# Performance work log

Measured on AMD Instinct MI355X. Metric: run time of the kernel, lower is better.

Reference implementation:

```python
import jax, jax.numpy as jnp
import numpy as np

E = 1024
H = 16
D = E // H
NUM_BUCKETS = 320
MAX_DISTANCE = 800


def _relative_positions_bucket(relative_positions):
    # relative_positions: int32 [T, S]
    num_buckets = NUM_BUCKETS // 2  # 160
    relative_buckets = (relative_positions > 0).astype(jnp.int32) * num_buckets
    rel = jnp.abs(relative_positions)
    max_exact = num_buckets // 2  # 80
    is_small = rel < max_exact
    rel_f = jnp.maximum(rel, 1).astype(jnp.float32)
    large = jnp.log(rel_f / max_exact) / np.log(MAX_DISTANCE / max_exact) * (num_buckets - max_exact)
    large = (max_exact + large).astype(jnp.int32)
    large = jnp.minimum(large, num_buckets - 1)
    relative_buckets = relative_buckets + jnp.where(is_small, rel, large)
    return relative_buckets


def setup_inputs() -> dict:
    key = jax.random.key(0)
    ks = jax.random.split(key, 12)
    B, T = 2, 2048
    s = 0.02
    return {
        "hidden_states": jax.random.normal(ks[0], (B, T, E), dtype=jnp.float32),
        "q_w": jax.random.normal(ks[1], (E, E), dtype=jnp.float32) * s,
        "q_b": jnp.zeros((E,), dtype=jnp.float32),
        "k_w": jax.random.normal(ks[2], (E, E), dtype=jnp.float32) * s,
        "k_b": jnp.zeros((E,), dtype=jnp.float32),
        "v_w": jax.random.normal(ks[3], (E, E), dtype=jnp.float32) * s,
        "v_b": jnp.zeros((E,), dtype=jnp.float32),
        "out_w": jax.random.normal(ks[4], (E, E), dtype=jnp.float32) * s,
        "out_b": jnp.zeros((E,), dtype=jnp.float32),
        "rel_embed": jax.random.normal(ks[5], (NUM_BUCKETS, H), dtype=jnp.float32) * s,
        "gru_const": jnp.ones((1, H, 1, 1), dtype=jnp.float32),
        "gru_w": jax.random.normal(ks[6], (8, D), dtype=jnp.float32) * s,
        "gru_b": jnp.zeros((8,), dtype=jnp.float32),
    }


def reference(hidden_states, q_w, q_b, k_w, k_b, v_w, v_b, out_w, out_b,
              rel_embed, gru_const, gru_w, gru_b):
    B, T, _ = hidden_states.shape
    scaling = D ** (-0.5)

    # --- relative position bias: [H, T, T] ---
    ctx = jnp.arange(T, dtype=jnp.int32)[:, None]
    mem = jnp.arange(T, dtype=jnp.int32)[None, :]
    buckets = _relative_positions_bucket(mem - ctx)          # [T, T]
    position_bias = rel_embed[buckets]                        # [T, T, H]
    position_bias = jnp.transpose(position_bias, (2, 0, 1))   # [H, T, T]

    # --- gate (gru_rel_pos): per (b, h, t) scalar ---
    gated = hidden_states.reshape(B, T, H, D).transpose(0, 2, 1, 3)  # [B,H,T,D]
    proj = jnp.einsum('bhtd,ed->bhte', gated, gru_w) + gru_b         # [B,H,T,8]
    proj = proj.reshape(B, H, T, 2, 4).sum(-1)                        # [B,H,T,2]
    gate = jax.nn.sigmoid(proj)
    gate_a = gate[..., 0:1]
    gate_b = gate[..., 1:2]
    gate_out = gate_a * (gate_b * gru_const - 1.0) + 2.0              # [B,H,T,1]
    gated_position_bias = gate_out * position_bias[None]              # [B,H,T,T]

    # --- attention (same math as F.multi_head_attention_forward eager path) ---
    q = (hidden_states @ q_w.T + q_b).reshape(B, T, H, D).transpose(0, 2, 1, 3) * scaling
    k = (hidden_states @ k_w.T + k_b).reshape(B, T, H, D).transpose(0, 2, 1, 3)
    v = (hidden_states @ v_w.T + v_b).reshape(B, T, H, D).transpose(0, 2, 1, 3)

    scores = jnp.einsum('bhtd,bhsd->bhts', q, k) + gated_position_bias
    attn = jax.nn.softmax(scores, axis=-1)
    ctx_out = jnp.einsum('bhts,bhsd->bhtd', attn, v)                  # [B,H,T,D]
    ctx_out = ctx_out.transpose(0, 2, 1, 3).reshape(B, T, E)
    return ctx_out @ out_w.T + out_b
```

## Files before the change

kernel.cpp:

```cpp
#include <hip/hip_runtime.h>
#include <hip/hip_bf16.h>
#include <math.h>

typedef __bf16 bf16;
typedef __bf16 bf16x4 __attribute__((ext_vector_type(4)));
typedef __bf16 bf16x8 __attribute__((ext_vector_type(8)));
typedef float  f32x4  __attribute__((ext_vector_type(4)));
typedef unsigned u32x2 __attribute__((ext_vector_type(2)));
typedef unsigned u32x4 __attribute__((ext_vector_type(4)));

#define T_SEQ 2048
#define E_DIM 1024
#define H_NUM 16
#define D_DIM 64
#define NDELTA 4095
#define LOG2E 1.4426950408889634f

__device__ __forceinline__ void gld16(const bf16* g, bf16* l) {
  __builtin_amdgcn_global_load_lds((__attribute__((address_space(1))) void*)(g),
                                   (__attribute__((address_space(3))) void*)(l), 16, 0, 0);
}

__device__ __forceinline__ void qswap(unsigned &a, unsigned &b) {
  u32x2 t  = __builtin_amdgcn_permlane32_swap(a, b, false, false);
  u32x2 t2 = __builtin_amdgcn_permlane16_swap(t[0], t[1], false, false);
  a = t2[0]; b = t2[1];
}

__global__ __launch_bounds__(256)
void cast_gate_kernel(const float* __restrict__ hs, bf16* __restrict__ hsb,
                      const float* __restrict__ gru_w, const float* __restrict__ gru_b,
                      const float* __restrict__ gconst, float* __restrict__ gate)
{
  __shared__ float w[512];
  const int tid = threadIdx.x;
  const int bt  = blockIdx.x;
  w[tid]       = gru_w[tid];
  w[tid + 256] = gru_w[tid + 256];
  __syncthreads();

  const int i = bt * 256 + tid;
  const float4 xv = reinterpret_cast<const float4*>(hs)[i];
  bf16x4 o;
  o[0] = (bf16)xv.x; o[1] = (bf16)xv.y; o[2] = (bf16)xv.z; o[3] = (bf16)xv.w;
  reinterpret_cast<bf16x4*>(hsb)[i] = o;

  const int h  = tid >> 4;
  const int d0 = (tid & 15) * 4;
  float acc[8];
#pragma unroll
  for (int e = 0; e < 8; e++) {
    acc[e] = xv.x * w[e*64+d0] + xv.y * w[e*64+d0+1]
           + xv.z * w[e*64+d0+2] + xv.w * w[e*64+d0+3];
  }
#pragma unroll
  for (int e = 0; e < 8; e++) {
    float v = acc[e];
    v += __shfl_xor(v, 1);
    v += __shfl_xor(v, 2);
    v += __shfl_xor(v, 4);
    v += __shfl_xor(v, 8);
    acc[e] = v;
  }
  if ((tid & 15) == 0) {
    float p0 = acc[0]+acc[1]+acc[2]+acc[3] + gru_b[0]+gru_b[1]+gru_b[2]+gru_b[3];
    float p1 = acc[4]+acc[5]+acc[6]+acc[7] + gru_b[4]+gru_b[5]+gru_b[6]+gru_b[7];
    float ga = 1.0f / (1.0f + expf(-p0));
    float gb = 1.0f / (1.0f + expf(-p1));
    float g = (ga * (gb * gconst[h] - 1.0f) + 2.0f) * LOG2E;
    int bb = bt >> 11;
    int t  = bt & (T_SEQ - 1);
    gate[((size_t)(bb * H_NUM + h)) * T_SEQ + t] = g;
  }
}

__global__ void cast_w_kernel(const float* __restrict__ q_w, const float* __restrict__ k_w,
                              const float* __restrict__ v_w, const float* __restrict__ o_w,
                              bf16* __restrict__ wcat, bf16* __restrict__ wob,
                              const float* __restrict__ rel_embed, float* __restrict__ pbt) {
  int sel = blockIdx.y;
  int tid = threadIdx.x;
  if (sel == 4) {
    int dd = blockIdx.x * 256 + tid;
    if (blockIdx.x >= 16 || dd >= NDELTA) return;
    int delta = dd - (T_SEQ - 1);
    int bucket = (delta > 0) ? 160 : 0;
    int rel = abs(delta);
    int v;
    if (rel < 80) {
      v = rel;
    } else {
      float rf = (float)(rel < 1 ? 1 : rel);
      float lf = logf(rf / 80.0f) * (80.0f / 2.302585092994046f);
      int lg = 80 + (int)lf;
      v = lg < 159 ? lg : 159;
    }
    bucket += v;
#pragma unroll
    for (int h = 0; h < H_NUM; h++)
      pbt[h * NDELTA + dd] = rel_embed[bucket * H_NUM + h];
    return;
  }
  int i = blockIdx.x * 256 + tid;
  const float* src = (sel == 0) ? q_w : (sel == 1) ? k_w : (sel == 2) ? v_w : o_w;
  bf16* dst = (sel < 3) ? (wcat + (size_t)sel * 1048576) : wob;
  const float4 v = reinterpret_cast<const float4*>(src)[i];
  bf16x4 o;
  o[0] = (bf16)v.x; o[1] = (bf16)v.y; o[2] = (bf16)v.z; o[3] = (bf16)v.w;
  reinterpret_cast<bf16x4*>(dst)[i] = o;
}

template<int MODE, int N_TOTAL>
__global__ __launch_bounds__(256)
void gemm2_kernel(const bf16* __restrict__ A, const bf16* __restrict__ W,
                  const float* __restrict__ b0, const float* __restrict__ b1,
                  const float* __restrict__ b2, float qalpha,
                  void* __restrict__ out0, void* __restrict__ out1, void* __restrict__ out2)
{
  __shared__ bf16 As[128 * 64];
  __shared__ bf16 Bs[128 * 64];
  const int tid  = threadIdx.x;
  const int lane = tid & 63;
  const int wave = tid >> 6;
  const int m0 = blockIdx.y * 128;
  const int n0 = blockIdx.x * 128;
  const int wm = (wave >> 1) * 64;
  const int wn = (wave & 1) * 64;
  const int qd = lane >> 4;
  const int lm = lane & 15;

  const int srow8  = lane >> 3;
  const int schunk = ((lane & 7) ^ srow8) * 8;
  const bf16* gA = A + (size_t)(m0 + wave * 32 + srow8) * 1024 + schunk;
  const bf16* gB = W + (size_t)(n0 + wave * 32 + srow8) * 1024 + schunk;
  bf16* lA = As + wave * 32 * 64;
  bf16* lB = Bs + wave * 32 * 64;

  f32x4 acc[4][4] = {};
  const int xs = lm & 7;

  for (int k0 = 0; k0 < 1024; k0 += 64) {
#pragma unroll
    for (int j = 0; j < 4; j++) {
      gld16(gA + (size_t)j * 8 * 1024 + k0, lA + j * 8 * 64);
      gld16(gB + (size_t)j * 8 * 1024 + k0, lB + j * 8 * 64);
    }
    __syncthreads();
    bf16x8 af[4][2], bfr[4][2];
#pragma unroll
    for (int i = 0; i < 4; i++) {
#pragma unroll
      for (int kk = 0; kk < 2; kk++) {
        af[i][kk]  = *(const bf16x8*)&As[(wm + i * 16 + lm) * 64 + (((kk * 4 + qd) ^ xs) * 8)];
        bfr[i][kk] = *(const bf16x8*)&Bs[(wn + i * 16 + lm) * 64 + (((kk * 4 + qd) ^ xs) * 8)];
      }
    }
#pragma unroll
    for (int kk = 0; kk < 2; kk++)
#pragma unroll
      for (int im = 0; im < 4; im++)
#pragma unroll
        for (int in = 0; in < 4; in++)
          acc[im][in] = __builtin_amdgcn_mfma_f32_16x16x32_bf16(af[im][kk], bfr[in][kk], acc[im][in], 0, 0, 0);
    __syncthreads();
  }

  const int seg = n0 >> 10;
  const float* bias = (MODE == 0) ? b0 : (seg == 0 ? b0 : (seg == 1 ? b1 : b2));
  const float alpha = (MODE == 1 && seg == 0) ? qalpha : 1.0f;

#pragma unroll
  for (int im = 0; im < 4; im++) {
#pragma unroll
    for (int in = 0; in < 4; in++) {
      const int n  = n0 + wn + in * 16 + lm;
      const int n1 = n & 1023;
      const float bv = bias[n1];
      const int mb = m0 + wm + im * 16 + qd * 4;
      if (MODE == 0) {
        float* o = (float*)out0;
#pragma unroll
        for (int r = 0; r < 4; r++)
          o[(size_t)(mb + r) * 1024 + n1] = acc[im][in][r] + bv;
      } else if (seg == 2) {
        const int bb = mb >> 11;
        const int t  = mb & 2047;
        bf16x4 pk;
#pragma unroll
        for (int r = 0; r < 4; r++) pk[r] = (bf16)(acc[im][in][r] + bv);
        *(bf16x4*)&((bf16*)out2)[((size_t)(bb * 1024 + n1)) * 2048 + t] = pk;
      } else {
        bf16* o = (bf16*)(seg == 0 ? out0 : out1);
#pragma unroll
        for (int r = 0; r < 4; r++)
          o[(size_t)(mb + r) * 1024 + n1] = (bf16)((acc[im][in][r] + bv) * alpha);
      }
    }
  }
}

__global__ __launch_bounds__(256)
void gemm_o_kernel(const bf16* __restrict__ A, const bf16* __restrict__ W,
                   const float* __restrict__ bias, float* __restrict__ out)
{
  __shared__ bf16 As[64 * 32];
  __shared__ bf16 Bs[128 * 32];
  const int tid  = threadIdx.x;
  const int lane = tid & 63;
  const int wave = tid >> 6;
  const int m0 = blockIdx.y * 64;
  const int n0 = blockIdx.x * 128;
  const int wm = (wave >> 1) * 32;
  const int wn = (wave & 1) * 64;
  const int qd = lane >> 4;
  const int lm = lane & 15;

  const int row4 = lane >> 2;
  const int col8 = (lane & 3) * 8;
  const bf16* gA0 = A + (size_t)(m0 + wave * 16 + row4) * 1024 + col8;
  const bf16* gB0 = W + (size_t)(n0 + wave * 32 + row4) * 1024 + col8;
  const bf16* gB1 = gB0 + (size_t)16 * 1024;
  bf16* lA0 = As + wave * 16 * 32;
  bf16* lB0 = Bs + (wave * 2 + 0) * 512;
  bf16* lB1 = Bs + (wave * 2 + 1) * 512;

  f32x4 acc[2][4] = {};

  for (int k0 = 0; k0 < 1024; k0 += 32) {
    gld16(gA0 + k0, lA0);
    gld16(gB0 + k0, lB0);
    gld16(gB1 + k0, lB1);
    __syncthreads();
    bf16x8 af[2], bfr[4];
#pragma unroll
    for (int i = 0; i < 2; i++)
      af[i]  = *(const bf16x8*)&As[(wm + i * 16 + lm) * 32 + qd * 8];
#pragma unroll
    for (int i = 0; i < 4; i++)
      bfr[i] = *(const bf16x8*)&Bs[(wn + i * 16 + lm) * 32 + qd * 8];
#pragma unroll
    for (int im = 0; im < 2; im++)
#pragma unroll
      for (int in = 0; in < 4; in++)
        acc[im][in] = __builtin_amdgcn_mfma_f32_16x16x32_bf16(af[im], bfr[in], acc[im][in], 0, 0, 0);
    __syncthreads();
  }

#pragma unroll
  for (int im = 0; im < 2; im++) {
#pragma unroll
    for (int in = 0; in < 4; in++) {
      const int n  = n0 + wn + in * 16 + lm;
      const float bv = bias[n];
      const int mb = m0 + wm + im * 16 + qd * 4;
#pragma unroll
      for (int r = 0; r < 4; r++)
        out[(size_t)(mb + r) * 1024 + n] = acc[im][in][r] + bv;
    }
  }
}

#define LK 72
__global__ __launch_bounds__(256)
void attn3_kernel(const bf16* __restrict__ Qg, const bf16* __restrict__ Kg,
                  const bf16* __restrict__ Vtg, const float* __restrict__ gate,
                  const float* __restrict__ pbt, bf16* __restrict__ ctx)
{
  __shared__ bf16 Ks[2][64 * LK];
  __shared__ bf16 Vs[2][64 * LK];
  __shared__ float pbs[2176];

  const int t0 = blockIdx.x * 128;
  const int h  = blockIdx.y;
  const int b  = blockIdx.z;
  const int tid  = threadIdx.x;
  const int lane = tid & 63;
  const int wave = tid >> 6;
  const int qd = lane >> 4;
  const int lm = lane & 15;

  for (int i = tid; i < 2176; i += 256) {
    int idx = i - t0 + 1920;
    pbs[i] = (idx >= 0 && idx < NDELTA) ? pbt[h * NDELTA + idx] : 0.0f;
  }

  bf16x8 qf[2][2];
  float g[2];
#pragma unroll
  for (int nb = 0; nb < 2; nb++) {
    const int q = t0 + wave * 32 + nb * 16 + lm;
    const bf16* qrow = Qg + (size_t)(b * T_SEQ + q) * E_DIM + h * D_DIM;
    qf[nb][0] = *(const bf16x8*)(qrow + qd * 8);
    qf[nb][1] = *(const bf16x8*)(qrow + 32 + qd * 8);
    g[nb] = gate[((size_t)(b * H_NUM + h)) * T_SEQ + q];
  }

  const int srow = tid >> 2;
  const int scol = (tid & 3) * 16;
  const bf16* kgp = Kg  + ((size_t)(b * T_SEQ) + srow) * E_DIM + h * D_DIM + scol;
  const bf16* vgp = Vtg + ((size_t)(b * 1024) + h * D_DIM + srow) * T_SEQ + scol;

  {
    bf16x8 a0 = *(const bf16x8*)kgp;
    bf16x8 a1 = *(const bf16x8*)(kgp + 8);
    bf16x8 c0 = *(const bf16x8*)vgp;
    bf16x8 c1 = *(const bf16x8*)(vgp + 8);
    *(bf16x8*)&Ks[0][srow * LK + scol]     = a0;
    *(bf16x8*)&Ks[0][srow * LK + scol + 8] = a1;
    *(bf16x8*)&Vs[0][srow * LK + scol]     = c0;
    *(bf16x8*)&Vs[0][srow * LK + scol + 8] = c1;
  }
  __syncthreads();

  f32x4 o[4][2] = {};
  float li[2] = {0.0f, 0.0f};

  for (int it = 0; it < T_SEQ / 64; it++) {
    const int s0 = it * 64;
    const int buf = it & 1;
    const bool more = (it + 1 < T_SEQ / 64);
    bf16x8 nk0, nk1, nv0, nv1;
    if (more) {
      const bf16* kn = kgp + (size_t)(s0 + 64) * E_DIM;
      const bf16* vn = vgp + (s0 + 64);
      nk0 = *(const bf16x8*)kn; nk1 = *(const bf16x8*)(kn + 8);
      nv0 = *(const bf16x8*)vn; nv1 = *(const bf16x8*)(vn + 8);
    }

    bf16x8 kf[4][2];
#pragma unroll
    for (int mb = 0; mb < 4; mb++) {
      kf[mb][0] = *(const bf16x8*)&Ks[buf][(16 * mb + lm) * LK + qd * 8];
      kf[mb][1] = *(const bf16x8*)&Ks[buf][(16 * mb + lm) * LK + 32 + qd * 8];
    }

    bf16x8 pf[2][2];
#pragma unroll
    for (int nb = 0; nb < 2; nb++) {
      f32x4 sc[4];
#pragma unroll
      for (int mb = 0; mb < 4; mb++) {
        f32x4 t = {};
        t = __builtin_amdgcn_mfma_f32_16x16x32_bf16(kf[mb][0], qf[nb][0], t, 0, 0, 0);
        t = __builtin_amdgcn_mfma_f32_16x16x32_bf16(kf[mb][1], qf[nb][1], t, 0, 0, 0);
        sc[mb] = t;
      }
      const int ib = s0 + 4 * qd + 127 - (wave * 32 + nb * 16 + lm);
      float rs = 0.0f;
      unsigned wlo[4], whi[4];
#pragma unroll
      for (int mb = 0; mb < 4; mb++) {
        bf16x4 pk;
#pragma unroll
        for (int r = 0; r < 4; r++) {
          float p = __builtin_amdgcn_exp2f(sc[mb][r] + g[nb] * pbs[ib + 16 * mb + r]);
          rs += p;
          pk[r] = (bf16)p;
        }
        u32x2 pw = __builtin_bit_cast(u32x2, pk);
        wlo[mb] = pw[0]; whi[mb] = pw[1];
      }
      li[nb] += rs;
      unsigned a0 = wlo[0], b0v = wlo[1], a1 = whi[0], b1v = whi[1];
      qswap(a0, b0v);
      qswap(a1, b1v);
      u32x4 h0; h0[0] = a0; h0[1] = a1; h0[2] = b0v; h0[3] = b1v;
      pf[nb][0] = __builtin_bit_cast(bf16x8, h0);
      unsigned c0 = wlo[2], d0v = wlo[3], c1 = whi[2], d1v = whi[3];
      qswap(c0, d0v);
      qswap(c1, d1v);
      u32x4 h1; h1[0] = c0; h1[1] = c1; h1[2] = d0v; h1[3] = d1v;
      pf[nb][1] = __builtin_bit_cast(bf16x8, h1);
    }

#pragma unroll
    for (int db = 0; db < 4; db++) {
      bf16x8 vf0 = *(const bf16x8*)&Vs[buf][(16 * db + lm) * LK + qd * 8];
      bf16x8 vf1 = *(const bf16x8*)&Vs[buf][(16 * db + lm) * LK + 32 + qd * 8];
#pragma unroll
      for (int nb = 0; nb < 2; nb++) {
        o[db][nb] = __builtin_amdgcn_mfma_f32_16x16x32_bf16(vf0, pf[nb][0], o[db][nb], 0, 0, 0);
        o[db][nb] = __builtin_amdgcn_mfma_f32_16x16x32_bf16(vf1, pf[nb][1], o[db][nb], 0, 0, 0);
      }
    }
    if (more) {
      *(bf16x8*)&Ks[buf ^ 1][srow * LK + scol]     = nk0;
      *(bf16x8*)&Ks[buf ^ 1][srow * LK + scol + 8] = nk1;
      *(bf16x8*)&Vs[buf ^ 1][srow * LK + scol]     = nv0;
      *(bf16x8*)&Vs[buf ^ 1][srow * LK + scol + 8] = nv1;
    }
    __syncthreads();
  }

#pragma unroll
  for (int nb = 0; nb < 2; nb++) {
    li[nb] += __shfl_xor(li[nb], 16);
    li[nb] += __shfl_xor(li[nb], 32);
  }
#pragma unroll
  for (int nb = 0; nb < 2; nb++) {
    const float inv = 1.0f / li[nb];
    const int q = t0 + wave * 32 + nb * 16 + lm;
    bf16* obase = ctx + (size_t)(b * T_SEQ + q) * E_DIM + h * D_DIM + 4 * qd;
#pragma unroll
    for (int db = 0; db < 4; db++) {
      bf16x4 ov;
      ov[0] = (bf16)(o[db][nb][0] * inv); ov[1] = (bf16)(o[db][nb][1] * inv);
      ov[2] = (bf16)(o[db][nb][2] * inv); ov[3] = (bf16)(o[db][nb][3] * inv);
      *(bf16x4*)&obase[16 * db] = ov;
    }
  }
}

extern "C" void kernel_launch(void* const* d_in, const int* in_sizes, int n_in,
                              void* d_out, int out_size, void* d_ws, size_t ws_size,
                              hipStream_t stream)
{
  const float* hs     = (const float*)d_in[0];
  const float* q_w    = (const float*)d_in[1];
  const float* q_b    = (const float*)d_in[2];
  const float* k_w    = (const float*)d_in[3];
  const float* k_b    = (const float*)d_in[4];
  const float* v_w    = (const float*)d_in[5];
  const float* v_b    = (const float*)d_in[6];
  const float* out_w  = (const float*)d_in[7];
  const float* out_b  = (const float*)d_in[8];
  const float* rel    = (const float*)d_in[9];
  const float* gconst = (const float*)d_in[10];
  const float* gru_w  = (const float*)d_in[11];
  const float* gru_b  = (const float*)d_in[12];

  char* p = (char*)d_ws;
  bf16* hsb  = (bf16*)p; p += (size_t)4096 * 1024 * 2;
  bf16* wcat = (bf16*)p; p += (size_t)3072 * 1024 * 2;
  bf16* wob  = (bf16*)p; p += (size_t)1024 * 1024 * 2;
  bf16* Qb   = (bf16*)p; p += (size_t)4096 * 1024 * 2;
  bf16* Kb   = (bf16*)p; p += (size_t)4096 * 1024 * 2;
  bf16* Vtb  = (bf16*)p; p += (size_t)2048 * 2048 * 2;
  bf16* ctxb = (bf16*)p; p += (size_t)4096 * 1024 * 2;
  float* gatep = (float*)p; p += (size_t)2 * H_NUM * T_SEQ * 4;
  float* pbt   = (float*)p; p += (size_t)H_NUM * NDELTA * 4;

  cast_gate_kernel<<<4096, 256, 0, stream>>>(hs, hsb, gru_w, gru_b, gconst, gatep);
  cast_w_kernel<<<dim3(1024, 5), 256, 0, stream>>>(q_w, k_w, v_w, out_w, wcat, wob, rel, pbt);

  const float qalpha = 0.125f * LOG2E;
  gemm2_kernel<1, 3072><<<dim3(24, 32), 256, 0, stream>>>(
      hsb, wcat, q_b, k_b, v_b, qalpha, Qb, Kb, Vtb);

  attn3_kernel<<<dim3(T_SEQ / 128, H_NUM, 2), 256, 0, stream>>>(Qb, Kb, Vtb, gatep, pbt, ctxb);

  gemm_o_kernel<<<dim3(8, 64), 256, 0, stream>>>(ctxb, wob, out_b, (float*)d_out);
}
```

Measured before the change: 219.7 us.

## Split attention KV loop across wave pairs and load K/V directly from global

The attention kernel doubles its block to 512 threads. Two groups of four waves each take alternating 64-key tiles and merge their partial outputs and row sums through shared memory at the end. The LDS double-buffered K/V staging and its per-iteration barriers are removed, and each wave now loads its MFMA operands straight from global memory (relying on L1/L2 for reuse). This removes the sync and LDS traffic and adds intra-block parallelism over the key dimension, at the cost of redundant global loads across waves and an exposed load latency with no explicit prefetch.

Result: slower. 289.1 us (+31.6%).

```diff
diff --git a/kernel.cpp b/kernel.cpp
--- a/kernel.cpp
+++ b/kernel.cpp
@@ -260,15 +260,14 @@
   }
 }
 
-#define LK 72
-__global__ __launch_bounds__(256)
+__global__ __launch_bounds__(512, 4)
 void attn3_kernel(const bf16* __restrict__ Qg, const bf16* __restrict__ Kg,
                   const bf16* __restrict__ Vtg, const float* __restrict__ gate,
                   const float* __restrict__ pbt, bf16* __restrict__ ctx)
 {
-  __shared__ bf16 Ks[2][64 * LK];
-  __shared__ bf16 Vs[2][64 * LK];
   __shared__ float pbs[2176];
+  __shared__ float oxf[4][64][36];
+  __shared__ float lixf[4][64][2];
 
   const int t0 = blockIdx.x * 128;
   const int h  = blockIdx.y;
@@ -276,10 +275,12 @@
   const int tid  = threadIdx.x;
   const int lane = tid & 63;
   const int wave = tid >> 6;
+  const int pw = wave & 3;
+  const int sh = wave >> 2;
   const int qd = lane >> 4;
   const int lm = lane & 15;
 
-  for (int i = tid; i < 2176; i += 256) {
+  for (int i = tid; i < 2176; i += 512) {
     int idx = i - t0 + 1920;
     pbs[i] = (idx >= 0 && idx < NDELTA) ? pbt[h * NDELTA + idx] : 0.0f;
   }
@@ -288,50 +289,36 @@
   float g[2];
 #pragma unroll
   for (int nb = 0; nb < 2; nb++) {
-    const int q = t0 + wave * 32 + nb * 16 + lm;
+    const int q = t0 + pw * 32 + nb * 16 + lm;
     const bf16* qrow = Qg + (size_t)(b * T_SEQ + q) * E_DIM + h * D_DIM;
     qf[nb][0] = *(const bf16x8*)(qrow + qd * 8);
     qf[nb][1] = *(const bf16x8*)(qrow + 32 + qd * 8);
     g[nb] = gate[((size_t)(b * H_NUM + h)) * T_SEQ + q];
   }
 
-  const int srow = tid >> 2;
-  const int scol = (tid & 3) * 16;
-  const bf16* kgp = Kg  + ((size_t)(b * T_SEQ) + srow) * E_DIM + h * D_DIM + scol;
-  const bf16* vgp = Vtg + ((size_t)(b * 1024) + h * D_DIM + srow) * T_SEQ + scol;
-
-  {
-    bf16x8 a0 = *(const bf16x8*)kgp;
-    bf16x8 a1 = *(const bf16x8*)(kgp + 8);
-    bf16x8 c0 = *(const bf16x8*)vgp;
-    bf16x8 c1 = *(const bf16x8*)(vgp + 8);
-    *(bf16x8*)&Ks[0][srow * LK + scol]     = a0;
-    *(bf16x8*)&Ks[0][srow * LK + scol + 8] = a1;
-    *(bf16x8*)&Vs[0][srow * LK + scol]     = c0;
-    *(bf16x8*)&Vs[0][srow * LK + scol + 8] = c1;
-  }
+  const bf16* krow[4];
+#pragma unroll
+  for (int mb = 0; mb < 4; mb++)
+    krow[mb] = Kg + ((size_t)(b * T_SEQ + 16 * mb + lm)) * E_DIM + h * D_DIM + qd * 8;
+  const bf16* vrow[4];
+#pragma unroll
+  for (int db = 0; db < 4; db++)
+    vrow[db] = Vtg + ((size_t)(b * 1024 + h * D_DIM + 16 * db + lm)) * T_SEQ + qd * 8;
+
   __syncthreads();
 
   f32x4 o[4][2] = {};
   float li[2] = {0.0f, 0.0f};
 
-  for (int it = 0; it < T_SEQ / 64; it++) {
+  for (int it = sh; it < T_SEQ / 64; it += 2) {
     const int s0 = it * 64;
-    const int buf = it & 1;
-    const bool more = (it + 1 < T_SEQ / 64);
-    bf16x8 nk0, nk1, nv0, nv1;
-    if (more) {
-      const bf16* kn = kgp + (size_t)(s0 + 64) * E_DIM;
-      const bf16* vn = vgp + (s0 + 64);
-      nk0 = *(const bf16x8*)kn; nk1 = *(const bf16x8*)(kn + 8);
-      nv0 = *(const bf16x8*)vn; nv1 = *(const bf16x8*)(vn + 8);
-    }
 
     bf16x8 kf[4][2];
 #pragma unroll
     for (int mb = 0; mb < 4; mb++) {
-      kf[mb][0] = *(const bf16x8*)&Ks[buf][(16 * mb + lm) * LK + qd * 8];
-      kf[mb][1] = *(const bf16x8*)&Ks[buf][(16 * mb + lm) * LK + 32 + qd * 8];
+      const bf16* kg = krow[mb] + (size_t)s0 * E_DIM;
+      kf[mb][0] = *(const bf16x8*)kg;
+      kf[mb][1] = *(const bf16x8*)(kg + 32);
     }
 
     bf16x8 pf[2][2];
@@ -345,7 +332,7 @@
         t = __builtin_amdgcn_mfma_f32_16x16x32_bf16(kf[mb][1], qf[nb][1], t, 0, 0, 0);
         sc[mb] = t;
       }
-      const int ib = s0 + 4 * qd + 127 - (wave * 32 + nb * 16 + lm);
+      const int ib = s0 + 4 * qd + 127 - (pw * 32 + nb * 16 + lm);
       float rs = 0.0f;
       unsigned wlo[4], whi[4];
 #pragma unroll
@@ -357,8 +344,8 @@
           rs += p;
           pk[r] = (bf16)p;
         }
-        u32x2 pw = __builtin_bit_cast(u32x2, pk);
-        wlo[mb] = pw[0]; whi[mb] = pw[1];
+        u32x2 pw2 = __builtin_bit_cast(u32x2, pk);
+        wlo[mb] = pw2[0]; whi[mb] = pw2[1];
       }
       li[nb] += rs;
       unsigned a0 = wlo[0], b0v = wlo[1], a1 = whi[0], b1v = whi[1];
@@ -375,39 +362,53 @@
 
 #pragma unroll
     for (int db = 0; db < 4; db++) {
-      bf16x8 vf0 = *(const bf16x8*)&Vs[buf][(16 * db + lm) * LK + qd * 8];
-      bf16x8 vf1 = *(const bf16x8*)&Vs[buf][(16 * db + lm) * LK + 32 + qd * 8];
+      const bf16* vg = vrow[db] + s0;
+      bf16x8 vf0 = *(const bf16x8*)vg;
+      bf16x8 vf1 = *(const bf16x8*)(vg + 32);
 #pragma unroll
       for (int nb = 0; nb < 2; nb++) {
         o[db][nb] = __builtin_amdgcn_mfma_f32_16x16x32_bf16(vf0, pf[nb][0], o[db][nb], 0, 0, 0);
         o[db][nb] = __builtin_amdgcn_mfma_f32_16x16x32_bf16(vf1, pf[nb][1], o[db][nb], 0, 0, 0);
       }
     }
-    if (more) {
-      *(bf16x8*)&Ks[buf ^ 1][srow * LK + scol]     = nk0;
-      *(bf16x8*)&Ks[buf ^ 1][srow * LK + scol + 8] = nk1;
-      *(bf16x8*)&Vs[buf ^ 1][srow * LK + scol]     = nv0;
-      *(bf16x8*)&Vs[buf ^ 1][srow * LK + scol + 8] = nv1;
-    }
-    __syncthreads();
-  }
-
-#pragma unroll
-  for (int nb = 0; nb < 2; nb++) {
-    li[nb] += __shfl_xor(li[nb], 16);
-    li[nb] += __shfl_xor(li[nb], 32);
-  }
-#pragma unroll
-  for (int nb = 0; nb < 2; nb++) {
-    const float inv = 1.0f / li[nb];
-    const int q = t0 + wave * 32 + nb * 16 + lm;
-    bf16* obase = ctx + (size_t)(b * T_SEQ + q) * E_DIM + h * D_DIM + 4 * qd;
-#pragma unroll
-    for (int db = 0; db < 4; db++) {
-      bf16x4 ov;
-      ov[0] = (bf16)(o[db][nb][0] * inv); ov[1] = (bf16)(o[db][nb][1] * inv);
-      ov[2] = (bf16)(o[db][nb][2] * inv); ov[3] = (bf16)(o[db][nb][3] * inv);
-      *(bf16x4*)&obase[16 * db] = ov;
+  }
+
+  if (sh == 1) {
+#pragma unroll
+    for (int db = 0; db < 4; db++)
+#pragma unroll
+      for (int nb = 0; nb < 2; nb++)
+        *(f32x4*)&oxf[pw][lane][(db * 2 + nb) * 4] = o[db][nb];
+    lixf[pw][lane][0] = li[0];
+    lixf[pw][lane][1] = li[1];
+  }
+  __syncthreads();
+  if (sh == 0) {
+#pragma unroll
+    for (int db = 0; db < 4; db++)
+#pragma unroll
+      for (int nb = 0; nb < 2; nb++)
+        o[db][nb] += *(const f32x4*)&oxf[pw][lane][(db * 2 + nb) * 4];
+    li[0] += lixf[pw][lane][0];
+    li[1] += lixf[pw][lane][1];
+
+#pragma unroll
+    for (int nb = 0; nb < 2; nb++) {
+      li[nb] += __shfl_xor(li[nb], 16);
+      li[nb] += __shfl_xor(li[nb], 32);
+    }
+#pragma unroll
+    for (int nb = 0; nb < 2; nb++) {
+      const float inv = 1.0f / li[nb];
+      const int q = t0 + pw * 32 + nb * 16 + lm;
+      bf16* obase = ctx + (size_t)(b * T_SEQ + q) * E_DIM + h * D_DIM + 4 * qd;
+#pragma unroll
+      for (int db = 0; db < 4; db++) {
+        bf16x4 ov;
+        ov[0] = (bf16)(o[db][nb][0] * inv); ov[1] = (bf16)(o[db][nb][1] * inv);
+        ov[2] = (bf16)(o[db][nb][2] * inv); ov[3] = (bf16)(o[db][nb][3] * inv);
+        *(bf16x4*)&obase[16 * db] = ov;
+      }
     }
   }
 }
@@ -448,7 +449,7 @@
   gemm2_kernel<1, 3072><<<dim3(24, 32), 256, 0, stream>>>(
       hsb, wcat, q_b, k_b, v_b, qalpha, Qb, Kb, Vtb);
 
-  attn3_kernel<<<dim3(T_SEQ / 128, H_NUM, 2), 256, 0, stream>>>(Qb, Kb, Vtb, gatep, pbt, ctxb);
+  attn3_kernel<<<dim3(T_SEQ / 128, H_NUM, 2), 512, 0, stream>>>(Qb, Kb, Vtb, gatep, pbt, ctxb);
 
   gemm_o_kernel<<<dim3(8, 64), 256, 0, stream>>>(ctxb, wob, out_b, (float*)d_out);
 }
```
